# Kernel tuning notes

Hardware: AMD Instinct MI355X
Metric: run time of the kernel (lower is better)

Reference implementation:

```python
import jax, jax.numpy as jnp
import numpy as np

N = 50000      # nodes
E = 800000     # edges
FIN = 128      # num_feature
EDIM = 16      # edge_dim
OUT = 64       # out_dim (per-head channels; concat=False averages heads)
H = 4          # heads
SCALE = 1.0 / float(np.sqrt(OUT))


def _layernorm(h, g, b):
    mu = h.mean(-1, keepdims=True)
    var = ((h - mu) ** 2).mean(-1, keepdims=True)
    return (h - mu) * jax.lax.rsqrt(var + 1e-5) * g + b


def _tconv(x, src, dst, ea, Wq, bq, Wk, bk, Wv, bv, We, Ws, bs):
    # PyG TransformerConv, concat=False, root_weight=True, eval mode (no dropout)
    n = x.shape[0]
    q = (x @ Wq + bq).reshape(n, H, OUT)[dst]   # [E,H,D] query at destination
    k = (x @ Wk + bk).reshape(n, H, OUT)[src]   # [E,H,D] key at source
    v = (x @ Wv + bv).reshape(n, H, OUT)[src]   # [E,H,D] value at source
    e = (ea @ We).reshape(-1, H, OUT)           # [E,H,D] edge embedding (no bias)
    logits = jnp.einsum('ehd,ehd->eh', q, k + e) * SCALE   # [E,H]
    # segment softmax over incoming edges of each destination node
    m = jax.lax.stop_gradient(jax.ops.segment_max(logits, dst, num_segments=n))
    a = jnp.exp(logits - m[dst])
    s = jax.ops.segment_sum(a, dst, num_segments=n)
    alpha = a / s[dst]                                     # [E,H]
    agg = jax.ops.segment_sum((v + e) * alpha[..., None], dst, num_segments=n)  # [N,H,D]
    return agg.mean(axis=1) + x @ Ws + bs      # concat=False -> head mean; + skip


def _forward(x, src, dst, ea, p1, p2, p3, g, b):
    h = x
    for p in (p1, p2, p3):
        h = jax.nn.gelu(_layernorm(_tconv(h, src, dst, ea, *p), g, b), approximate=False)
    return h


def setup_inputs() -> dict:
    key = jax.random.key(0)
    ks = iter(jax.random.split(key, 64))
    def nrm(shp, s=0.05):
        return jax.random.normal(next(ks), shp, jnp.float32) * s
    inp = {
        'x': nrm((N, FIN), 1.0),
        'edge_index': jax.random.randint(next(ks), (2, E), 0, N),
        'edge_attr': nrm((E, EDIM), 1.0),
    }
    for l, fin in ((1, FIN), (2, OUT), (3, OUT)):
        inp[f'Wq{l}'] = nrm((fin, H * OUT)); inp[f'bq{l}'] = jnp.zeros((H * OUT,), jnp.float32)
        inp[f'Wk{l}'] = nrm((fin, H * OUT)); inp[f'bk{l}'] = jnp.zeros((H * OUT,), jnp.float32)
        inp[f'Wv{l}'] = nrm((fin, H * OUT)); inp[f'bv{l}'] = jnp.zeros((H * OUT,), jnp.float32)
        inp[f'We{l}'] = nrm((EDIM, H * OUT))
        inp[f'Ws{l}'] = nrm((fin, OUT)); inp[f'bs{l}'] = jnp.zeros((OUT,), jnp.float32)
    inp['ln_g'] = jnp.ones((OUT,), jnp.float32)
    inp['ln_b'] = jnp.zeros((OUT,), jnp.float32)
    return inp


def reference(x, edge_index, edge_attr,
              Wq1, bq1, Wk1, bk1, Wv1, bv1, We1, Ws1, bs1,
              Wq2, bq2, Wk2, bk2, Wv2, bv2, We2, Ws2, bs2,
              Wq3, bq3, Wk3, bk3, Wv3, bv3, We3, Ws3, bs3,
              ln_g, ln_b):
    src, dst = edge_index[0], edge_index[1]
    p1 = (Wq1, bq1, Wk1, bk1, Wv1, bv1, We1, Ws1, bs1)
    p2 = (Wq2, bq2, Wk2, bk2, Wv2, bv2, We2, Ws2, bs2)
    p3 = (Wq3, bq3, Wk3, bk3, Wv3, bv3, We3, Ws3, bs3)
    return _forward(x, src, dst, edge_attr, p1, p2, p3, ln_g, ln_b)
```

## Files before the change

kernel.cpp:

```cpp
#include <hip/hip_runtime.h>
#include <hip/hip_bf16.h>
#include <math.h>

#define NNODES 50000
#define NEDGES 800000
#define HD     256
#define CW     640

typedef __hip_bfloat16 bf16;
typedef unsigned short u16;
typedef unsigned char  u8;
typedef unsigned int   u32;
typedef __attribute__((ext_vector_type(8))) short bf16x8;
typedef __attribute__((ext_vector_type(4))) float f32x4;
typedef __attribute__((ext_vector_type(2))) float f32x2;

__device__ __forceinline__ float lo16f(u32 u) { return __uint_as_float(u << 16); }
__device__ __forceinline__ float hi16f(u32 u) { return __uint_as_float(u & 0xFFFF0000u); }
__device__ __forceinline__ short f2s(float v) { __hip_bfloat16 h = __float2bfloat16(v); return *(short*)&h; }

__global__ void hist_kernel(const int* __restrict__ dst, int* __restrict__ deg, int E) {
    int e = blockIdx.x * 256 + threadIdx.x;
    if (e < E) atomicAdd(&deg[dst[e]], 1);
}

__global__ void scanA(const int* __restrict__ deg, int* __restrict__ locincl,
                      int* __restrict__ blocksum, int n) {
    int tid = threadIdx.x;
    int i = blockIdx.x * 256 + tid;
    int v = (i < n) ? deg[i] : 0;
    int lane = tid & 63, w = tid >> 6;
    int s = v;
    #pragma unroll
    for (int off = 1; off < 64; off <<= 1) {
        int t = __shfl_up(s, off);
        if (lane >= off) s += t;
    }
    __shared__ int wsum[4];
    if (lane == 63) wsum[w] = s;
    __syncthreads();
    for (int ww = 0; ww < w; ww++) s += wsum[ww];
    if (i < n) locincl[i] = s;
    if (tid == 255) blocksum[blockIdx.x] = s;
}

__global__ void scanB(const int* __restrict__ blocksum, int* __restrict__ blockoff,
                      int nb, int* __restrict__ rowptr, int n) {
    int tid = threadIdx.x;
    int v = (tid < nb) ? blocksum[tid] : 0;
    int lane = tid & 63, w = tid >> 6;
    int s = v;
    #pragma unroll
    for (int off = 1; off < 64; off <<= 1) {
        int t = __shfl_up(s, off);
        if (lane >= off) s += t;
    }
    __shared__ int wsum[4];
    if (lane == 63) wsum[w] = s;
    __syncthreads();
    for (int ww = 0; ww < w; ww++) s += wsum[ww];
    if (tid < nb) blockoff[tid] = s - v;
    if (tid == 255) rowptr[n] = s;
}

__global__ void scanC(const int* __restrict__ deg, const int* __restrict__ locincl,
                      const int* __restrict__ blockoff,
                      int* __restrict__ rowptr, int* __restrict__ cursor, int n) {
    int i = blockIdx.x * 256 + threadIdx.x;
    if (i < n) {
        int ex = locincl[i] - deg[i] + blockoff[blockIdx.x];
        rowptr[i] = ex;
        cursor[i] = ex;
    }
}

__global__ void scatter_kernel(const int* __restrict__ src, const int* __restrict__ dst,
                               int* __restrict__ cursor, int2* __restrict__ csr2, int E) {
    int e = blockIdx.x * 256 + threadIdx.x;
    if (e < E) {
        int d = dst[e];
        int p = atomicAdd(&cursor[d], 1);
        csr2[p] = make_int2(src[e], e);
    }
}

__global__ void wqwe_kernel(const float* __restrict__ Wq, const float* __restrict__ bq,
                            const float* __restrict__ We, float* __restrict__ out, int FIN) {
    int c = blockIdx.x;
    int t = threadIdx.x;
    int h = t >> 4, j = t & 15;
    const float* qrow = (c == FIN) ? bq : (Wq + (size_t)c * HD);
    float s = 0.f;
    #pragma unroll 8
    for (int d = 0; d < 64; d++) s += qrow[h * 64 + d] * We[j * HD + h * 64 + d];
    out[c * 64 + t] = s;
}

__global__ void pack640(const float* __restrict__ Wq, const float* __restrict__ bq,
                        const float* __restrict__ wqwe,
                        const float* __restrict__ Wv, const float* __restrict__ bv,
                        const float* __restrict__ Ws, const float* __restrict__ bs,
                        bf16* __restrict__ Wc, float* __restrict__ b, int K) {
    int n = blockIdx.x, c = threadIdx.x;
    float v, bb;
    if (n < 256)      { v = Wq[(size_t)c * 256 + n];       bb = bq[n]; }
    else if (n < 320) { v = wqwe[c * 64 + (n - 256)];      bb = wqwe[K * 64 + (n - 256)]; }
    else if (n < 576) { v = Wv[(size_t)c * 256 + (n - 320)]; bb = bv[n - 320]; }
    else              { v = Ws[(size_t)c * 64 + (n - 576)];  bb = bs[n - 576]; }
    Wc[(size_t)n * K + c] = __float2bfloat16(v);
    if (c == 0) b[n] = bb;
}

__global__ void packK(const float* __restrict__ Wk, const float* __restrict__ bk,
                      bf16* __restrict__ Wc, float* __restrict__ b, int K) {
    int n = blockIdx.x, c = threadIdx.x;
    Wc[(size_t)n * K + c] = __float2bfloat16(Wk[(size_t)c * 256 + n]);
    if (c == 0) b[n] = bk[n];
}

template<typename TA, bool OUT8>
__global__ void __launch_bounds__(256) gemm_mfma(
    const TA* __restrict__ A, int K,
    const bf16* __restrict__ Wc, const float* __restrict__ bias,
    int M, void* __restrict__ outp, int ldo)
{
    __shared__ short Al[64 * 40];
    __shared__ short Bl[64 * 40];
    int m0 = blockIdx.x * 64, n0 = blockIdx.y * 64;
    int tid = threadIdx.x;
    int w = tid >> 6, lane = tid & 63;
    int lr = tid >> 2, lc = (tid & 3) * 8;
    f32x4 acc[4] = {};

    for (int k0 = 0; k0 < K; k0 += 32) {
        __syncthreads();
        {
            int m = m0 + lr;
            uint4 val = make_uint4(0, 0, 0, 0);
            if (m < M) {
                if constexpr (sizeof(TA) == 4) {
                    const float4* ap = (const float4*)((const float*)A + (size_t)m * K + k0 + lc);
                    float4 f0 = ap[0], f1 = ap[1];
                    union { short s[8]; uint4 u; } t;
                    t.s[0] = f2s(f0.x); t.s[1] = f2s(f0.y); t.s[2] = f2s(f0.z); t.s[3] = f2s(f0.w);
                    t.s[4] = f2s(f1.x); t.s[5] = f2s(f1.y); t.s[6] = f2s(f1.z); t.s[7] = f2s(f1.w);
                    val = t.u;
                } else {
                    val = *(const uint4*)((const u16*)A + (size_t)m * K + k0 + lc);
                }
            }
            *(uint4*)&Al[lr * 40 + lc] = val;
        }
        *(uint4*)&Bl[lr * 40 + lc] = *(const uint4*)((const u16*)Wc + (size_t)(n0 + lr) * K + k0 + lc);
        __syncthreads();

        int am = lane & 15, aq = lane >> 4;
        bf16x8 af = *(const bf16x8*)&Al[(w * 16 + am) * 40 + aq * 8];
        #pragma unroll
        for (int t = 0; t < 4; t++) {
            bf16x8 bfr = *(const bf16x8*)&Bl[(t * 16 + am) * 40 + aq * 8];
            acc[t] = __builtin_amdgcn_mfma_f32_16x16x32_bf16(af, bfr, acc[t], 0, 0, 0);
        }
    }
    int cl = lane & 15, rq = lane >> 4;
    #pragma unroll
    for (int t = 0; t < 4; t++) {
        int c = n0 + t * 16 + cl;
        float bv = bias[c];
        #pragma unroll
        for (int r = 0; r < 4; r++) {
            int m = m0 + w * 16 + rq * 4 + r;
            if (m < M) {
                float v = acc[t][r] + bv;
                if constexpr (OUT8) {
                    int pk = __builtin_amdgcn_cvt_pk_fp8_f32(v, v, 0, false);
                    ((u8*)outp)[(size_t)m * ldo + c] = (u8)(pk & 0xFF);
                } else {
                    ((bf16*)outp)[(size_t)m * ldo + c] = __float2bfloat16(v);
                }
            }
        }
    }
}

__device__ __forceinline__ void edge_accum(
    int s, int eid,
    const u16* __restrict__ comb, const u8* __restrict__ k8, const float* __restrict__ eattr,
    int coff, int j16,
    float qf0, float qf1, float qf2, float qf3, float qwe_r,
    float& ss, float& av0, float& av1, float& av2, float& av3, float& ae)
{
    u32  kw = *(const u32*)(k8 + s * 256 + coff);
    uint2 vw = *(const uint2*)(comb + s * CW + 320 + coff);
    float ea = eattr[eid * 16 + j16];
    f32x2 k01 = __builtin_amdgcn_cvt_pk_f32_fp8(kw, false);
    f32x2 k23 = __builtin_amdgcn_cvt_pk_f32_fp8(kw, true);
    float part = qf0 * k01[0] + qf1 * k01[1] + qf2 * k23[0] + qf3 * k23[1] + qwe_r * ea;
    part += __shfl_xor(part, 1);
    part += __shfl_xor(part, 2);
    part += __shfl_xor(part, 4);
    part += __shfl_xor(part, 8);
    float alpha = __expf(part * 0.125f);
    ss += alpha;
    ae += alpha * ea;
    av0 += alpha * lo16f(vw.x); av1 += alpha * hi16f(vw.x);
    av2 += alpha * lo16f(vw.y); av3 += alpha * hi16f(vw.y);
}

__global__ void __launch_bounds__(256) node_fused(
    const int* __restrict__ rowptr, const int2* __restrict__ csr2,
    const float* __restrict__ eattr, const u16* __restrict__ comb,
    const u8* __restrict__ k8, const float* __restrict__ We,
    const float* __restrict__ lng, const float* __restrict__ lnb,
    bf16* __restrict__ outB, float* __restrict__ outF)
{
    int tid = threadIdx.x, w = tid >> 6, lane = tid & 63;
    int n = blockIdx.x * 4 + w;
    int hg = lane >> 4, j16 = lane & 15, coff = 4 * lane;
    __shared__ float sAV[4][256];
    __shared__ float sAE[4][64];

    const u16* crow = comb + (size_t)n * CW;
    uint2 qv = *(const uint2*)(crow + coff);
    float qf0 = lo16f(qv.x), qf1 = hi16f(qv.x), qf2 = lo16f(qv.y), qf3 = hi16f(qv.y);
    float qwe_r = __uint_as_float((u32)crow[256 + lane] << 16);

    int e0 = rowptr[n], e1 = rowptr[n + 1];
    float ss = 0.f, av0 = 0.f, av1 = 0.f, av2 = 0.f, av3 = 0.f, ae = 0.f;

    for (int base = e0; base < e1; base += 64) {
        int cnt = e1 - base; if (cnt > 64) cnt = 64;
        int2 meta = make_int2(0, 0);
        if (lane < cnt) meta = csr2[base + lane];
        int i = 0;
        for (; i + 3 < cnt; i += 4) {
            int s0 = __builtin_amdgcn_readlane(meta.x, i);
            int q0 = __builtin_amdgcn_readlane(meta.y, i);
            int s1 = __builtin_amdgcn_readlane(meta.x, i + 1);
            int q1 = __builtin_amdgcn_readlane(meta.y, i + 1);
            int s2 = __builtin_amdgcn_readlane(meta.x, i + 2);
            int q2 = __builtin_amdgcn_readlane(meta.y, i + 2);
            int s3 = __builtin_amdgcn_readlane(meta.x, i + 3);
            int q3 = __builtin_amdgcn_readlane(meta.y, i + 3);
            edge_accum(s0, q0, comb, k8, eattr, coff, j16, qf0, qf1, qf2, qf3, qwe_r, ss, av0, av1, av2, av3, ae);
            edge_accum(s1, q1, comb, k8, eattr, coff, j16, qf0, qf1, qf2, qf3, qwe_r, ss, av0, av1, av2, av3, ae);
            edge_accum(s2, q2, comb, k8, eattr, coff, j16, qf0, qf1, qf2, qf3, qwe_r, ss, av0, av1, av2, av3, ae);
            edge_accum(s3, q3, comb, k8, eattr, coff, j16, qf0, qf1, qf2, qf3, qwe_r, ss, av0, av1, av2, av3, ae);
        }
        for (; i < cnt; ++i) {
            int s0 = __builtin_amdgcn_readlane(meta.x, i);
            int q0 = __builtin_amdgcn_readlane(meta.y, i);
            edge_accum(s0, q0, comb, k8, eattr, coff, j16, qf0, qf1, qf2, qf3, qwe_r, ss, av0, av1, av2, av3, ae);
        }
    }

    float inv = (ss > 0.f) ? 1.f / ss : 0.f;
    *(float4*)&sAV[w][coff] = make_float4(av0 * inv, av1 * inv, av2 * inv, av3 * inv);
    sAE[w][lane] = ae * inv;

    int d = lane;
    float val = 0.f;
    #pragma unroll
    for (int h = 0; h < 4; h++) {
        float xv = sAV[w][h * 64 + d];
        #pragma unroll
        for (int j = 0; j < 16; j++) xv += sAE[w][h * 16 + j] * We[j * HD + h * 64 + d];
        val += xv;
    }
    val = val * 0.25f + __uint_as_float((u32)crow[576 + d] << 16);

    float m = val;
    #pragma unroll
    for (int off = 1; off < 64; off <<= 1) m += __shfl_xor(m, off);
    m *= (1.f / 64.f);
    float diff = val - m;
    float vr = diff * diff;
    #pragma unroll
    for (int off = 1; off < 64; off <<= 1) vr += __shfl_xor(vr, off);
    vr *= (1.f / 64.f);
    float y = diff * rsqrtf(vr + 1e-5f) * lng[d] + lnb[d];
    float ge = 0.5f * y * (1.f + erff(y * 0.70710678118654752f));
    if (outF) outF[(size_t)n * 64 + d] = ge;
    else      outB[(size_t)n * 64 + d] = __float2bfloat16(ge);
}

extern "C" void kernel_launch(void* const* d_in, const int* in_sizes, int n_in,
                              void* d_out, int out_size, void* d_ws, size_t ws_size,
                              hipStream_t stream)
{
    const float* x     = (const float*)d_in[0];
    const int*   eidx  = (const int*)d_in[1];
    const float* eattr = (const float*)d_in[2];
    struct P { const float *Wq,*bq,*Wk,*bk,*Wv,*bv,*We,*Ws,*bs; };
    P p[3];
    for (int l = 0; l < 3; l++) {
        int base = 3 + l * 9;
        p[l].Wq = (const float*)d_in[base + 0]; p[l].bq = (const float*)d_in[base + 1];
        p[l].Wk = (const float*)d_in[base + 2]; p[l].bk = (const float*)d_in[base + 3];
        p[l].Wv = (const float*)d_in[base + 4]; p[l].bv = (const float*)d_in[base + 5];
        p[l].We = (const float*)d_in[base + 6];
        p[l].Ws = (const float*)d_in[base + 7]; p[l].bs = (const float*)d_in[base + 8];
    }
    const float* lng = (const float*)d_in[30];
    const float* lnb = (const float*)d_in[31];

    char* ws = (char*)d_ws;
    size_t off = 0;
    auto alloc = [&](size_t bytes) { void* pp = ws + off; off += (bytes + 255) & ~(size_t)255; return pp; };
    int*   rowptr   = (int*)  alloc((NNODES + 1) * 4);
    int*   cursor   = (int*)  alloc(NNODES * 4);
    int*   deg      = (int*)  alloc(NNODES * 4);
    int*   blocksum = (int*)  alloc(256 * 4);
    int*   blockoff = (int*)  alloc(256 * 4);
    int2*  csr2     = (int2*) alloc((size_t)NEDGES * 8);
    bf16*  hbuf     = (bf16*) alloc((size_t)NNODES * 64 * 2);
    bf16*  comb     = (bf16*) alloc((size_t)NNODES * CW * 2);
    u8*    k8       = (u8*)   alloc((size_t)NNODES * 256);
    float* wqwe     = (float*)alloc((size_t)129 * 64 * 4);
    bf16*  Wc640    = (bf16*) alloc((size_t)640 * 128 * 2);
    bf16*  WcK      = (bf16*) alloc((size_t)256 * 128 * 2);
    float* b640     = (float*)alloc(640 * 4);
    float* bK       = (float*)alloc(256 * 4);
    (void)ws_size;

    const int* srcArr = eidx;
    const int* dstArr = eidx + NEDGES;

    int NB = (NNODES + 255) / 256;
    (void)hipMemsetAsync(deg, 0, NNODES * 4, stream);
    hist_kernel<<<(NEDGES + 255) / 256, 256, 0, stream>>>(dstArr, deg, NEDGES);
    scanA<<<NB, 256, 0, stream>>>(deg, cursor, blocksum, NNODES);
    scanB<<<1, 256, 0, stream>>>(blocksum, blockoff, NB, rowptr, NNODES);
    scanC<<<NB, 256, 0, stream>>>(deg, cursor, blockoff, rowptr, cursor, NNODES);
    scatter_kernel<<<(NEDGES + 255) / 256, 256, 0, stream>>>(srcArr, dstArr, cursor, csr2, NEDGES);

    int gm = (NNODES + 63) / 64;
    int fins[3] = {128, 64, 64};

    const void* hin = x;
    for (int l = 0; l < 3; l++) {
        int FIN = fins[l];
        wqwe_kernel<<<FIN + 1, 64, 0, stream>>>(p[l].Wq, p[l].bq, p[l].We, wqwe, FIN);
        pack640<<<640, FIN, 0, stream>>>(p[l].Wq, p[l].bq, wqwe, p[l].Wv, p[l].bv,
                                         p[l].Ws, p[l].bs, Wc640, b640, FIN);
        packK<<<256, FIN, 0, stream>>>(p[l].Wk, p[l].bk, WcK, bK, FIN);
        if (l == 0) {
            gemm_mfma<float, false><<<dim3(gm, 10), 256, 0, stream>>>((const float*)hin, FIN, Wc640, b640, NNODES, comb, CW);
            gemm_mfma<float, true> <<<dim3(gm, 4),  256, 0, stream>>>((const float*)hin, FIN, WcK,   bK,   NNODES, k8, 256);
        } else {
            gemm_mfma<bf16, false><<<dim3(gm, 10), 256, 0, stream>>>((const bf16*)hin, FIN, Wc640, b640, NNODES, comb, CW);
            gemm_mfma<bf16, true> <<<dim3(gm, 4),  256, 0, stream>>>((const bf16*)hin, FIN, WcK,   bK,   NNODES, k8, 256);
        }
        node_fused<<<NNODES / 4, 256, 0, stream>>>(rowptr, csr2, eattr, (const u16*)comb, k8,
            p[l].We, lng, lnb, (l == 2) ? nullptr : hbuf, (l == 2) ? (float*)d_out : nullptr);
        hin = hbuf;
    }
}
```

Baseline: 760.2 us.

## Fuse weight packing and dual GEMMs into single per-layer kernels; DPP reductions

Merges the wqwe, pack640 and packK kernels into one pack_all kernel that packs Q, Q·We, V, skip and K weights into a single 896-column matrix. It also replaces the two tiled GEMMs with one gemm_fused kernel, which keeps each row's A fragments in registers and loops over 14 column chunks with XOR-swizzled LDS. Output stores are vectorised (packed bf16 pairs and packed fp8x4). In the edge loop, shuffle-xor reductions become DPP adds and addressing uses 32-bit byte offsets. The aim is fewer launches, no re-reading of A per column tile, and cheaper stores, at the cost of one block doing all columns, which means fewer blocks and less parallelism.

```diff
diff --git a/kernel.cpp b/kernel.cpp
--- a/kernel.cpp
+++ b/kernel.cpp
@@ -6,6 +6,7 @@
 #define NEDGES 800000
 #define HD     256
 #define CW     640
+#define NTOT   896
 
 typedef __hip_bfloat16 bf16;
 typedef unsigned short u16;
@@ -18,6 +19,12 @@
 __device__ __forceinline__ float lo16f(u32 u) { return __uint_as_float(u << 16); }
 __device__ __forceinline__ float hi16f(u32 u) { return __uint_as_float(u & 0xFFFF0000u); }
 __device__ __forceinline__ short f2s(float v) { __hip_bfloat16 h = __float2bfloat16(v); return *(short*)&h; }
+
+template<int CTRL>
+__device__ __forceinline__ float dppadd(float x) {
+    int t = __builtin_amdgcn_update_dpp(0, __float_as_int(x), CTRL, 0xF, 0xF, true);
+    return x + __int_as_float(t);
+}
 
 __global__ void hist_kernel(const int* __restrict__ dst, int* __restrict__ deg, int E) {
     int e = blockIdx.x * 256 + threadIdx.x;
@@ -84,122 +91,124 @@
     }
 }
 
-__global__ void wqwe_kernel(const float* __restrict__ Wq, const float* __restrict__ bq,
-                            const float* __restrict__ We, float* __restrict__ out, int FIN) {
-    int c = blockIdx.x;
-    int t = threadIdx.x;
-    int h = t >> 4, j = t & 15;
-    const float* qrow = (c == FIN) ? bq : (Wq + (size_t)c * HD);
-    float s = 0.f;
-    #pragma unroll 8
-    for (int d = 0; d < 64; d++) s += qrow[h * 64 + d] * We[j * HD + h * 64 + d];
-    out[c * 64 + t] = s;
-}
-
-__global__ void pack640(const float* __restrict__ Wq, const float* __restrict__ bq,
-                        const float* __restrict__ wqwe,
-                        const float* __restrict__ Wv, const float* __restrict__ bv,
-                        const float* __restrict__ Ws, const float* __restrict__ bs,
-                        bf16* __restrict__ Wc, float* __restrict__ b, int K) {
+__global__ void pack_all(const float* __restrict__ Wq, const float* __restrict__ bq,
+                         const float* __restrict__ Wk, const float* __restrict__ bk,
+                         const float* __restrict__ Wv, const float* __restrict__ bv,
+                         const float* __restrict__ We,
+                         const float* __restrict__ Ws, const float* __restrict__ bs,
+                         bf16* __restrict__ Wc, float* __restrict__ b, int K) {
     int n = blockIdx.x, c = threadIdx.x;
     float v, bb;
-    if (n < 256)      { v = Wq[(size_t)c * 256 + n];       bb = bq[n]; }
-    else if (n < 320) { v = wqwe[c * 64 + (n - 256)];      bb = wqwe[K * 64 + (n - 256)]; }
+    if (n < 256)      { v = Wq[(size_t)c * 256 + n];         bb = bq[n]; }
+    else if (n < 320) {
+        int t = n - 256, h = t >> 4, j = t & 15;
+        float s = 0.f, sb = 0.f;
+        #pragma unroll 8
+        for (int d = 0; d < 64; d++) {
+            float wv = We[j * HD + h * 64 + d];
+            s += Wq[(size_t)c * 256 + h * 64 + d] * wv;
+            sb += bq[h * 64 + d] * wv;
+        }
+        v = s; bb = sb;
+    }
     else if (n < 576) { v = Wv[(size_t)c * 256 + (n - 320)]; bb = bv[n - 320]; }
-    else              { v = Ws[(size_t)c * 64 + (n - 576)];  bb = bs[n - 576]; }
+    else if (n < 640) { v = Ws[(size_t)c * 64  + (n - 576)]; bb = bs[n - 576]; }
+    else              { v = Wk[(size_t)c * 256 + (n - 640)]; bb = bk[n - 640]; }
     Wc[(size_t)n * K + c] = __float2bfloat16(v);
     if (c == 0) b[n] = bb;
 }
 
-__global__ void packK(const float* __restrict__ Wk, const float* __restrict__ bk,
-                      bf16* __restrict__ Wc, float* __restrict__ b, int K) {
-    int n = blockIdx.x, c = threadIdx.x;
-    Wc[(size_t)n * K + c] = __float2bfloat16(Wk[(size_t)c * 256 + n]);
-    if (c == 0) b[n] = bk[n];
-}
-
-template<typename TA, bool OUT8>
-__global__ void __launch_bounds__(256) gemm_mfma(
-    const TA* __restrict__ A, int K,
-    const bf16* __restrict__ Wc, const float* __restrict__ bias,
-    int M, void* __restrict__ outp, int ldo)
+template<typename TA, int K>
+__global__ void __launch_bounds__(256) gemm_fused(
+    const TA* __restrict__ A, const bf16* __restrict__ Wc, const float* __restrict__ bias,
+    bf16* __restrict__ comb, u8* __restrict__ k8)
 {
-    __shared__ short Al[64 * 40];
-    __shared__ short Bl[64 * 40];
-    int m0 = blockIdx.x * 64, n0 = blockIdx.y * 64;
-    int tid = threadIdx.x;
-    int w = tid >> 6, lane = tid & 63;
-    int lr = tid >> 2, lc = (tid & 3) * 8;
-    f32x4 acc[4] = {};
-
-    for (int k0 = 0; k0 < K; k0 += 32) {
+    constexpr int KS  = K / 32;
+    constexpr int CPR = K / 8;
+    __shared__ short Bl[64 * K];
+    int tid = threadIdx.x, w = tid >> 6, lane = tid & 63;
+    int cl = lane & 15, aq = lane >> 4;
+    int m = blockIdx.x * 64 + w * 16 + cl;
+    int rowc = (m < NNODES) ? m : (NNODES - 1);
+
+    bf16x8 af[KS];
+    if constexpr (sizeof(TA) == 4) {
+        const float* ar = (const float*)A + (size_t)rowc * K;
+        #pragma unroll
+        for (int ks = 0; ks < KS; ks++) {
+            const float4* ap = (const float4*)(ar + ks * 32 + aq * 8);
+            float4 f0 = ap[0], f1 = ap[1];
+            union { short s[8]; bf16x8 v; } t;
+            t.s[0] = f2s(f0.x); t.s[1] = f2s(f0.y); t.s[2] = f2s(f0.z); t.s[3] = f2s(f0.w);
+            t.s[4] = f2s(f1.x); t.s[5] = f2s(f1.y); t.s[6] = f2s(f1.z); t.s[7] = f2s(f1.w);
+            af[ks] = t.v;
+        }
+    } else {
+        const u16* ar = (const u16*)A + (size_t)rowc * K;
+        #pragma unroll
+        for (int ks = 0; ks < KS; ks++) af[ks] = *(const bf16x8*)(ar + ks * 32 + aq * 8);
+    }
+
+    for (int chunk = 0; chunk < 14; chunk++) {
+        int n0 = chunk * 64;
         __syncthreads();
-        {
-            int m = m0 + lr;
-            uint4 val = make_uint4(0, 0, 0, 0);
-            if (m < M) {
-                if constexpr (sizeof(TA) == 4) {
-                    const float4* ap = (const float4*)((const float*)A + (size_t)m * K + k0 + lc);
-                    float4 f0 = ap[0], f1 = ap[1];
-                    union { short s[8]; uint4 u; } t;
-                    t.s[0] = f2s(f0.x); t.s[1] = f2s(f0.y); t.s[2] = f2s(f0.z); t.s[3] = f2s(f0.w);
-                    t.s[4] = f2s(f1.x); t.s[5] = f2s(f1.y); t.s[6] = f2s(f1.z); t.s[7] = f2s(f1.w);
-                    val = t.u;
+        #pragma unroll
+        for (int p = 0; p < CPR / 4; p++) {
+            int slot = tid + p * 256;
+            int row = slot / CPR, j = slot % CPR;
+            *(uint4*)&Bl[row * K + ((j ^ (row & 7)) << 3)] =
+                *(const uint4*)((const u16*)Wc + (size_t)(n0 + row) * K + (j << 3));
+        }
+        __syncthreads();
+
+        f32x4 acc[4] = {};
+        #pragma unroll
+        for (int t = 0; t < 4; t++) {
+            #pragma unroll
+            for (int ks = 0; ks < KS; ks++) {
+                int g = ((ks * 4 + aq) ^ (cl & 7)) << 3;
+                bf16x8 bfr = *(const bf16x8*)&Bl[(t * 16 + cl) * K + g];
+                acc[t] = __builtin_amdgcn_mfma_f32_16x16x32_bf16(bfr, af[ks], acc[t], 0, 0, 0);
+            }
+        }
+
+        if (m < NNODES) {
+            #pragma unroll
+            for (int t = 0; t < 4; t++) {
+                float4 bv = *(const float4*)&bias[n0 + t * 16 + aq * 4];
+                float v0 = acc[t][0] + bv.x, v1 = acc[t][1] + bv.y;
+                float v2 = acc[t][2] + bv.z, v3 = acc[t][3] + bv.w;
+                if (chunk < 10) {
+                    u32 lo = (u32)(u16)f2s(v0) | ((u32)(u16)f2s(v1) << 16);
+                    u32 hi = (u32)(u16)f2s(v2) | ((u32)(u16)f2s(v3) << 16);
+                    *(uint2*)((u16*)comb + (size_t)m * CW + n0 + t * 16 + aq * 4) = make_uint2(lo, hi);
                 } else {
-                    val = *(const uint4*)((const u16*)A + (size_t)m * K + k0 + lc);
+                    u32 pk = __builtin_amdgcn_cvt_pk_fp8_f32(v0, v1, 0, false);
+                    pk = __builtin_amdgcn_cvt_pk_fp8_f32(v2, v3, pk, true);
+                    *(u32*)(k8 + (size_t)m * 256 + (n0 - 640) + t * 16 + aq * 4) = pk;
                 }
             }
-            *(uint4*)&Al[lr * 40 + lc] = val;
-        }
-        *(uint4*)&Bl[lr * 40 + lc] = *(const uint4*)((const u16*)Wc + (size_t)(n0 + lr) * K + k0 + lc);
-        __syncthreads();
-
-        int am = lane & 15, aq = lane >> 4;
-        bf16x8 af = *(const bf16x8*)&Al[(w * 16 + am) * 40 + aq * 8];
-        #pragma unroll
-        for (int t = 0; t < 4; t++) {
-            bf16x8 bfr = *(const bf16x8*)&Bl[(t * 16 + am) * 40 + aq * 8];
-            acc[t] = __builtin_amdgcn_mfma_f32_16x16x32_bf16(af, bfr, acc[t], 0, 0, 0);
-        }
-    }
-    int cl = lane & 15, rq = lane >> 4;
-    #pragma unroll
-    for (int t = 0; t < 4; t++) {
-        int c = n0 + t * 16 + cl;
-        float bv = bias[c];
-        #pragma unroll
-        for (int r = 0; r < 4; r++) {
-            int m = m0 + w * 16 + rq * 4 + r;
-            if (m < M) {
-                float v = acc[t][r] + bv;
-                if constexpr (OUT8) {
-                    int pk = __builtin_amdgcn_cvt_pk_fp8_f32(v, v, 0, false);
-                    ((u8*)outp)[(size_t)m * ldo + c] = (u8)(pk & 0xFF);
-                } else {
-                    ((bf16*)outp)[(size_t)m * ldo + c] = __float2bfloat16(v);
-                }
-            }
         }
     }
 }
 
 __device__ __forceinline__ void edge_accum(
-    int s, int eid,
-    const u16* __restrict__ comb, const u8* __restrict__ k8, const float* __restrict__ eattr,
-    int coff, int j16,
+    u32 s, u32 eid,
+    const char* __restrict__ comb_b, const char* __restrict__ k8_b, const char* __restrict__ eattr_b,
+    u32 koff, u32 voff, u32 eoff,
     float qf0, float qf1, float qf2, float qf3, float qwe_r,
     float& ss, float& av0, float& av1, float& av2, float& av3, float& ae)
 {
-    u32  kw = *(const u32*)(k8 + s * 256 + coff);
-    uint2 vw = *(const uint2*)(comb + s * CW + 320 + coff);
-    float ea = eattr[eid * 16 + j16];
+    u32   kw = *(const u32*)  (k8_b   + ((s << 8) + koff));
+    uint2 vw = *(const uint2*)(comb_b + (s * 1280u + voff));
+    float ea = *(const float*)(eattr_b + ((eid << 6) + eoff));
     f32x2 k01 = __builtin_amdgcn_cvt_pk_f32_fp8(kw, false);
     f32x2 k23 = __builtin_amdgcn_cvt_pk_f32_fp8(kw, true);
     float part = qf0 * k01[0] + qf1 * k01[1] + qf2 * k23[0] + qf3 * k23[1] + qwe_r * ea;
-    part += __shfl_xor(part, 1);
-    part += __shfl_xor(part, 2);
-    part += __shfl_xor(part, 4);
-    part += __shfl_xor(part, 8);
+    part = dppadd<0xB1>(part);
+    part = dppadd<0x4E>(part);
+    part = dppadd<0x141>(part);
+    part = dppadd<0x140>(part);
     float alpha = __expf(part * 0.125f);
     ss += alpha;
     ae += alpha * ea;
@@ -225,6 +234,13 @@
     float qf0 = lo16f(qv.x), qf1 = hi16f(qv.x), qf2 = lo16f(qv.y), qf3 = hi16f(qv.y);
     float qwe_r = __uint_as_float((u32)crow[256 + lane] << 16);
 
+    const char* comb_b  = (const char*)comb;
+    const char* k8_b    = (const char*)k8;
+    const char* eattr_b = (const char*)eattr;
+    u32 koff = (u32)coff;
+    u32 voff = 640u + ((u32)coff << 1);
+    u32 eoff = (u32)j16 << 2;
+
     int e0 = rowptr[n], e1 = rowptr[n + 1];
     float ss = 0.f, av0 = 0.f, av1 = 0.f, av2 = 0.f, av3 = 0.f, ae = 0.f;
 
@@ -234,23 +250,23 @@
         if (lane < cnt) meta = csr2[base + lane];
         int i = 0;
         for (; i + 3 < cnt; i += 4) {
-            int s0 = __builtin_amdgcn_readlane(meta.x, i);
-            int q0 = __builtin_amdgcn_readlane(meta.y, i);
-            int s1 = __builtin_amdgcn_readlane(meta.x, i + 1);
-            int q1 = __builtin_amdgcn_readlane(meta.y, i + 1);
-            int s2 = __builtin_amdgcn_readlane(meta.x, i + 2);
-            int q2 = __builtin_amdgcn_readlane(meta.y, i + 2);
-            int s3 = __builtin_amdgcn_readlane(meta.x, i + 3);
-            int q3 = __builtin_amdgcn_readlane(meta.y, i + 3);
-            edge_accum(s0, q0, comb, k8, eattr, coff, j16, qf0, qf1, qf2, qf3, qwe_r, ss, av0, av1, av2, av3, ae);
-            edge_accum(s1, q1, comb, k8, eattr, coff, j16, qf0, qf1, qf2, qf3, qwe_r, ss, av0, av1, av2, av3, ae);
-            edge_accum(s2, q2, comb, k8, eattr, coff, j16, qf0, qf1, qf2, qf3, qwe_r, ss, av0, av1, av2, av3, ae);
-            edge_accum(s3, q3, comb, k8, eattr, coff, j16, qf0, qf1, qf2, qf3, qwe_r, ss, av0, av1, av2, av3, ae);
+            u32 s0 = __builtin_amdgcn_readlane(meta.x, i);
+            u32 q0 = __builtin_amdgcn_readlane(meta.y, i);
+            u32 s1 = __builtin_amdgcn_readlane(meta.x, i + 1);
+            u32 q1 = __builtin_amdgcn_readlane(meta.y, i + 1);
+            u32 s2 = __builtin_amdgcn_readlane(meta.x, i + 2);
+            u32 q2 = __builtin_amdgcn_readlane(meta.y, i + 2);
+            u32 s3 = __builtin_amdgcn_readlane(meta.x, i + 3);
+            u32 q3 = __builtin_amdgcn_readlane(meta.y, i + 3);
+            edge_accum(s0, q0, comb_b, k8_b, eattr_b, koff, voff, eoff, qf0, qf1, qf2, qf3, qwe_r, ss, av0, av1, av2, av3, ae);
+            edge_accum(s1, q1, comb_b, k8_b, eattr_b, koff, voff, eoff, qf0, qf1, qf2, qf3, qwe_r, ss, av0, av1, av2, av3, ae);
+            edge_accum(s2, q2, comb_b, k8_b, eattr_b, koff, voff, eoff, qf0, qf1, qf2, qf3, qwe_r, ss, av0, av1, av2, av3, ae);
+            edge_accum(s3, q3, comb_b, k8_b, eattr_b, koff, voff, eoff, qf0, qf1, qf2, qf3, qwe_r, ss, av0, av1, av2, av3, ae);
         }
         for (; i < cnt; ++i) {
-            int s0 = __builtin_amdgcn_readlane(meta.x, i);
-            int q0 = __builtin_amdgcn_readlane(meta.y, i);
-            edge_accum(s0, q0, comb, k8, eattr, coff, j16, qf0, qf1, qf2, qf3, qwe_r, ss, av0, av1, av2, av3, ae);
+            u32 s0 = __builtin_amdgcn_readlane(meta.x, i);
+            u32 q0 = __builtin_amdgcn_readlane(meta.y, i);
+            edge_accum(s0, q0, comb_b, k8_b, eattr_b, koff, voff, eoff, qf0, qf1, qf2, qf3, qwe_r, ss, av0, av1, av2, av3, ae);
         }
     }
 
@@ -316,11 +332,8 @@
     bf16*  hbuf     = (bf16*) alloc((size_t)NNODES * 64 * 2);
     bf16*  comb     = (bf16*) alloc((size_t)NNODES * CW * 2);
     u8*    k8       = (u8*)   alloc((size_t)NNODES * 256);
-    float* wqwe     = (float*)alloc((size_t)129 * 64 * 4);
-    bf16*  Wc640    = (bf16*) alloc((size_t)640 * 128 * 2);
-    bf16*  WcK      = (bf16*) alloc((size_t)256 * 128 * 2);
-    float* b640     = (float*)alloc(640 * 4);
-    float* bK       = (float*)alloc(256 * 4);
+    bf16*  Wc       = (bf16*) alloc((size_t)NTOT * 128 * 2);
+    float* b896     = (float*)alloc(NTOT * 4);
     (void)ws_size;
 
     const int* srcArr = eidx;
@@ -340,17 +353,11 @@
     const void* hin = x;
     for (int l = 0; l < 3; l++) {
         int FIN = fins[l];
-        wqwe_kernel<<<FIN + 1, 64, 0, stream>>>(p[l].Wq, p[l].bq, p[l].We, wqwe, FIN);
-        pack640<<<640, FIN, 0, stream>>>(p[l].Wq, p[l].bq, wqwe, p[l].Wv, p[l].bv,
-                                         p[l].Ws, p[l].bs, Wc640, b640, FIN);
-        packK<<<256, FIN, 0, stream>>>(p[l].Wk, p[l].bk, WcK, bK, FIN);
-        if (l == 0) {
-            gemm_mfma<float, false><<<dim3(gm, 10), 256, 0, stream>>>((const float*)hin, FIN, Wc640, b640, NNODES, comb, CW);
-            gemm_mfma<float, true> <<<dim3(gm, 4),  256, 0, stream>>>((const float*)hin, FIN, WcK,   bK,   NNODES, k8, 256);
-        } else {
-            gemm_mfma<bf16, false><<<dim3(gm, 10), 256, 0, stream>>>((const bf16*)hin, FIN, Wc640, b640, NNODES, comb, CW);
-            gemm_mfma<bf16, true> <<<dim3(gm, 4),  256, 0, stream>>>((const bf16*)hin, FIN, WcK,   bK,   NNODES, k8, 256);
-        }
+        pack_all<<<NTOT, FIN, 0, stream>>>(p[l].Wq, p[l].bq, p[l].Wk, p[l].bk,
+                                           p[l].Wv, p[l].bv, p[l].We, p[l].Ws, p[l].bs,
+                                           Wc, b896, FIN);
+        if (l == 0) gemm_fused<float, 128><<<gm, 256, 0, stream>>>((const float*)hin, Wc, b896, comb, k8);
+        else        gemm_fused<bf16,  64><<<gm, 256, 0, stream>>>((const bf16*)hin,  Wc, b896, comb, k8);
         node_fused<<<NNODES / 4, 256, 0, stream>>>(rowptr, csr2, eattr, (const u16*)comb, k8,
             p[l].We, lng, lnb, (l == 2) ? nullptr : hbuf, (l == 2) ? (float*)d_out : nullptr);
         hin = hbuf;
```

Measured after the change: 688.5 us. 9.4% less time.
